# Kernel optimization log

Hardware: AMD Instinct MI355X
Metric: run time of the kernel (lower is better)

Reference implementation:

```python
import jax, jax.numpy as jnp
import numpy as np

IN_F = 4096
OUT_F = 4096
SPARSITY = 0.1
BATCH = 8192
TOTAL_PERM = max(IN_F, OUT_F)
DIAG_LEN = min(IN_F, OUT_F)
K = int(np.ceil((1.0 - SPARSITY) * IN_F * OUT_F / DIAG_LEN))  # 3687


def setup_inputs() -> dict:
    key = jax.random.key(0)
    k1, k2, k3 = jax.random.split(key, 3)
    x = jax.random.normal(k1, (BATCH, IN_F), dtype=jnp.float32)
    # kaiming_uniform_(a=sqrt(5)) on (TOTAL_PERM, DIAG_LEN): bound = 1/sqrt(fan_in)
    bound = 1.0 / np.sqrt(DIAG_LEN)
    V = jax.random.uniform(k2, (TOTAL_PERM, DIAG_LEN), jnp.float32, -bound, bound)
    # original init is constant 1/in_features; add small noise so soft top-k is non-trivial
    alpha = 1.0 / IN_F + 0.01 * jax.random.normal(k3, (TOTAL_PERM,), jnp.float32)
    return {"x": x, "V": V, "alpha": alpha}


def _compute_weight(V, alpha):
    # soft top-k: k * softmax(alpha / T), T=1, clamped to [0,1]; softmax > 0 so all
    # total_permutations diagonals participate (matches torch.nonzero behavior).
    a_topk = jnp.clip(K * jax.nn.softmax(alpha), 0.0, 1.0)  # [TOTAL_PERM]
    Vs = V * a_topk[:, None]  # [TOTAL_PERM, DIAG_LEN]
    d = jnp.arange(DIAG_LEN)
    # out_features >= in_features branch: diagonal i occupies rows (i+j)%out, cols j
    rows = (jnp.arange(TOTAL_PERM)[:, None] + d[None, :]) % OUT_F  # [N, D]
    cols = jnp.broadcast_to(d[None, :], (TOTAL_PERM, DIAG_LEN))
    W = jnp.zeros((OUT_F, IN_F), dtype=V.dtype).at[rows, cols].add(Vs)
    return W


def reference(x, V, alpha):
    W = _compute_weight(V, alpha)  # [OUT_F, IN_F]
    return x @ W.T  # F.linear(x, W)
```

## Files before the change

### kernel.cpp

```cpp
#include <hip/hip_runtime.h>

#define IN_F 4096
#define OUT_F 4096
#define BATCH 8192
#define KTOP 3687.0f

typedef float f32x4 __attribute__((ext_vector_type(4)));
typedef short bf16x8 __attribute__((ext_vector_type(8)));
typedef unsigned short ushort8 __attribute__((ext_vector_type(8)));

typedef __attribute__((address_space(1))) void gvoid;
typedef __attribute__((address_space(3))) void lvoid;

__device__ __forceinline__ unsigned short f2bf(float f) {
    unsigned int u = __float_as_uint(f);
    u += 0x7fff + ((u >> 16) & 1);
    return (unsigned short)(u >> 16);
}

__global__ __launch_bounds__(256) void atopk_kernel(const float* __restrict__ alpha,
                                                    float* __restrict__ atopk) {
    __shared__ float smax[4], ssum[4];
    int tid = threadIdx.x;
    float m = -1e30f;
    for (int i = tid; i < OUT_F; i += 256) m = fmaxf(m, alpha[i]);
    for (int o = 1; o < 64; o <<= 1) m = fmaxf(m, __shfl_xor(m, o));
    if ((tid & 63) == 0) smax[tid >> 6] = m;
    __syncthreads();
    m = fmaxf(fmaxf(smax[0], smax[1]), fmaxf(smax[2], smax[3]));
    float s = 0.f;
    for (int i = tid; i < OUT_F; i += 256) s += expf(alpha[i] - m);
    for (int o = 1; o < 64; o <<= 1) s += __shfl_xor(s, o);
    if ((tid & 63) == 0) ssum[tid >> 6] = s;
    __syncthreads();
    s = ssum[0] + ssum[1] + ssum[2] + ssum[3];
    float inv = 1.0f / s;
    for (int i = tid; i < OUT_F; i += 256) {
        float v = KTOP * expf(alpha[i] - m) * inv;
        atopk[i] = fminf(fmaxf(v, 0.0f), 1.0f);
    }
}

__global__ __launch_bounds__(256) void build_w_kernel(const float* __restrict__ V,
                                                      const float* __restrict__ atopk,
                                                      unsigned short* __restrict__ W) {
    int tx = threadIdx.x & 63;
    int ty = threadIdx.x >> 6;
    int c  = blockIdx.x * 64 + tx;
    int r0 = blockIdx.y * 64;
    #pragma unroll
    for (int it = 0; it < 16; ++it) {
        int r = r0 + it * 4 + ty;
        int s = (r - c) & (OUT_F - 1);
        float v = V[s * IN_F + c] * atopk[s];
        W[(long)r * IN_F + c] = f2bf(v);
    }
}

__global__ __launch_bounds__(256) void cvt_x_kernel(const float* __restrict__ x,
                                                    unsigned short* __restrict__ xb) {
    long i = ((long)blockIdx.x * 256 + threadIdx.x) * 8;
    const float* p = x + i;
    ushort8 o;
    #pragma unroll
    for (int j = 0; j < 8; ++j) o[j] = f2bf(p[j]);
    *(ushort8*)(xb + i) = o;
}

__global__ __launch_bounds__(256) void gemm_kernel(const unsigned short* __restrict__ A,
                                                   const unsigned short* __restrict__ Bt,
                                                   float* __restrict__ C) {
    __shared__ unsigned short As[2][128][32];
    __shared__ unsigned short Bs[2][128][32];

    const int tid = threadIdx.x;
    const int w = tid >> 6;
    const int l = tid & 63;
    const int wr = w >> 1, wc = w & 1;
    const int bn = blockIdx.x, bm = blockIdx.y;

    f32x4 acc[4][4] = {};

    const int srow = l >> 2;
    const int scol = (l & 3) * 8;
    const unsigned short* Abase = A  + ((long)bm * 128) * IN_F;
    const unsigned short* Bbase = Bt + ((long)bn * 128) * IN_F;

    const int lr = l & 15;
    const int lk = (l >> 4) * 8;

    for (int k0 = 0; k0 < IN_F; k0 += 64) {
        #pragma unroll
        for (int i = 0; i < 4; ++i) {
            int q = w * 4 + i;
            int h = q >> 3;
            int row = (q & 7) * 16 + srow;
            int kc = k0 + h * 32 + scol;
            __builtin_amdgcn_global_load_lds((gvoid*)(Abase + (long)row * IN_F + kc),
                                             (lvoid*)(&As[0][0][0] + q * 512), 16, 0, 0);
            __builtin_amdgcn_global_load_lds((gvoid*)(Bbase + (long)row * IN_F + kc),
                                             (lvoid*)(&Bs[0][0][0] + q * 512), 16, 0, 0);
        }
        __syncthreads();

        #pragma unroll
        for (int kk = 0; kk < 2; ++kk) {
            bf16x8 af[4], bfr[4];
            #pragma unroll
            for (int m = 0; m < 4; ++m)
                af[m] = *(const bf16x8*)(&As[kk][wr * 64 + m * 16 + lr][lk]);
            #pragma unroll
            for (int n = 0; n < 4; ++n)
                bfr[n] = *(const bf16x8*)(&Bs[kk][wc * 64 + n * 16 + lr][lk]);
            #pragma unroll
            for (int m = 0; m < 4; ++m)
                #pragma unroll
                for (int n = 0; n < 4; ++n)
                    acc[m][n] = __builtin_amdgcn_mfma_f32_16x16x32_bf16(af[m], bfr[n], acc[m][n], 0, 0, 0);
        }
        __syncthreads();
    }

    const long r0 = (long)bm * 128 + wr * 64;
    const int  c0 = bn * 128 + wc * 64;
    const int  rq = (l >> 4) * 4;
    #pragma unroll
    for (int m = 0; m < 4; ++m)
        #pragma unroll
        for (int n = 0; n < 4; ++n)
            #pragma unroll
            for (int v = 0; v < 4; ++v)
                C[(r0 + m * 16 + rq + v) * OUT_F + (c0 + n * 16 + lr)] = acc[m][n][v];
}

extern "C" void kernel_launch(void* const* d_in, const int* in_sizes, int n_in,
                              void* d_out, int out_size, void* d_ws, size_t ws_size,
                              hipStream_t stream) {
    const float* x     = (const float*)d_in[0];
    const float* V     = (const float*)d_in[1];
    const float* alpha = (const float*)d_in[2];
    float* out = (float*)d_out;

    char* ws = (char*)d_ws;
    float* atopk      = (float*)ws;
    unsigned short* W  = (unsigned short*)(ws + 16384);
    unsigned short* Xb = (unsigned short*)(ws + 16384 + (size_t)OUT_F * IN_F * 2);

    atopk_kernel<<<1, 256, 0, stream>>>(alpha, atopk);
    build_w_kernel<<<dim3(IN_F / 64, OUT_F / 64), 256, 0, stream>>>(V, atopk, W);
    cvt_x_kernel<<<(BATCH * IN_F / 8) / 256, 256, 0, stream>>>(x, Xb);
    gemm_kernel<<<dim3(OUT_F / 128, BATCH / 128), 256, 0, stream>>>(Xb, W, out);
}
```

Baseline: 634.4 us.

## Enlarge GEMM tiles to 256x256 with swizzled LDS and double-buffered prefetch

The GEMM moves from 128x128 tiles with 4 waves to 256x256 tiles with 8 waves and a K-step of 64. It uses an XOR-swizzled LDS layout to avoid bank conflicts, double-buffered asynchronous global-to-LDS loads with explicit vmcnt waits, and s_setprio around the MFMA bursts. The build_w kernel also stages a diagonal band of V in shared memory so its reads are coalesced instead of strided. The bigger tiles cut global traffic per FLOP and overlap loads with compute, at the cost of heavy LDS use (128KB) and register pressure from 32 accumulators, which limits occupancy.

Measured after the change: 547.9 us. -13.6%, faster.

```diff
diff --git a/kernel.cpp b/kernel.cpp
--- a/kernel.cpp
+++ b/kernel.cpp
@@ -4,6 +4,7 @@
 #define OUT_F 4096
 #define BATCH 8192
 #define KTOP 3687.0f
+#define NT (IN_F / 64)
 
 typedef float f32x4 __attribute__((ext_vector_type(4)));
 typedef short bf16x8 __attribute__((ext_vector_type(8)));
@@ -44,16 +45,29 @@
 __global__ __launch_bounds__(256) void build_w_kernel(const float* __restrict__ V,
                                                       const float* __restrict__ atopk,
                                                       unsigned short* __restrict__ W) {
-    int tx = threadIdx.x & 63;
-    int ty = threadIdx.x >> 6;
-    int c  = blockIdx.x * 64 + tx;
-    int r0 = blockIdx.y * 64;
+    __shared__ float Vl[128][64];
+    __shared__ float al[128];
+    const int t = threadIdx.x;
+    const int tx = t & 63, ty = t >> 6;
+    const int c0 = blockIdx.x * 64;
+    const int r0 = blockIdx.y * 64;
+    const int s_base = (r0 - c0 - 63 + 4096) & 4095;
+
+    #pragma unroll
+    for (int i = 0; i < 32; ++i) {
+        int sr = i * 4 + ty;
+        int gs = (s_base + sr) & 4095;
+        Vl[sr][tx] = V[(long)gs * IN_F + c0 + tx];
+    }
+    if (t < 128) al[t] = atopk[(s_base + t) & 4095];
+    __syncthreads();
+
     #pragma unroll
     for (int it = 0; it < 16; ++it) {
-        int r = r0 + it * 4 + ty;
-        int s = (r - c) & (OUT_F - 1);
-        float v = V[s * IN_F + c] * atopk[s];
-        W[(long)r * IN_F + c] = f2bf(v);
+        int ry = it * 4 + ty;
+        int si = ry - tx + 63;
+        float v = Vl[si][tx] * al[si];
+        W[(long)(r0 + ry) * IN_F + c0 + tx] = f2bf(v);
     }
 }
 
@@ -67,70 +81,126 @@
     *(ushort8*)(xb + i) = o;
 }
 
-__global__ __launch_bounds__(256) void gemm_kernel(const unsigned short* __restrict__ A,
-                                                   const unsigned short* __restrict__ Bt,
-                                                   float* __restrict__ C) {
-    __shared__ unsigned short As[2][128][32];
-    __shared__ unsigned short Bs[2][128][32];
+__global__ __launch_bounds__(512, 2) void gemm_kernel(const unsigned short* __restrict__ A,
+                                                      const unsigned short* __restrict__ Bt,
+                                                      float* __restrict__ C) {
+    __shared__ unsigned short As[2][256][64];
+    __shared__ unsigned short Bs[2][256][64];
 
     const int tid = threadIdx.x;
-    const int w = tid >> 6;
-    const int l = tid & 63;
-    const int wr = w >> 1, wc = w & 1;
+    const int l  = tid & 63;
+    const int w  = tid >> 6;
+    const int wr = w >> 2;
+    const int wc = w & 3;
+    const int lr = l & 15;
+    const int kq = l >> 4;
+    const int swz = (lr & 7) << 3;
+
     const int bn = blockIdx.x, bm = blockIdx.y;
 
-    f32x4 acc[4][4] = {};
-
-    const int srow = l >> 2;
-    const int scol = (l & 3) * 8;
-    const unsigned short* Abase = A  + ((long)bm * 128) * IN_F;
-    const unsigned short* Bbase = Bt + ((long)bn * 128) * IN_F;
-
-    const int lr = l & 15;
-    const int lk = (l >> 4) * 8;
-
-    for (int k0 = 0; k0 < IN_F; k0 += 64) {
-        #pragma unroll
-        for (int i = 0; i < 4; ++i) {
-            int q = w * 4 + i;
-            int h = q >> 3;
-            int row = (q & 7) * 16 + srow;
-            int kc = k0 + h * 32 + scol;
-            __builtin_amdgcn_global_load_lds((gvoid*)(Abase + (long)row * IN_F + kc),
-                                             (lvoid*)(&As[0][0][0] + q * 512), 16, 0, 0);
-            __builtin_amdgcn_global_load_lds((gvoid*)(Bbase + (long)row * IN_F + kc),
-                                             (lvoid*)(&Bs[0][0][0] + q * 512), 16, 0, 0);
-        }
-        __syncthreads();
-
-        #pragma unroll
-        for (int kk = 0; kk < 2; ++kk) {
-            bf16x8 af[4], bfr[4];
-            #pragma unroll
-            for (int m = 0; m < 4; ++m)
-                af[m] = *(const bf16x8*)(&As[kk][wr * 64 + m * 16 + lr][lk]);
-            #pragma unroll
-            for (int n = 0; n < 4; ++n)
-                bfr[n] = *(const bf16x8*)(&Bs[kk][wc * 64 + n * 16 + lr][lk]);
-            #pragma unroll
-            for (int m = 0; m < 4; ++m)
-                #pragma unroll
-                for (int n = 0; n < 4; ++n)
-                    acc[m][n] = __builtin_amdgcn_mfma_f32_16x16x32_bf16(af[m], bfr[n], acc[m][n], 0, 0, 0);
-        }
-        __syncthreads();
-    }
-
-    const long r0 = (long)bm * 128 + wr * 64;
-    const int  c0 = bn * 128 + wc * 64;
-    const int  rq = (l >> 4) * 4;
-    #pragma unroll
-    for (int m = 0; m < 4; ++m)
+    const unsigned short* Ab = A  + (long)bm * 256 * IN_F;
+    const unsigned short* Bb = Bt + (long)bn * 256 * IN_F;
+
+    const int srow = tid >> 3;
+    const int schunk = (tid & 7) ^ (srow & 7);
+    const int sdst = tid * 8;
+
+    f32x4 acc[8][4] = {};
+
+#define STAGE(kt, b) do {                                                          \
+    const unsigned short* ga_ = Ab + (long)(kt) * 64;                              \
+    const unsigned short* gb_ = Bb + (long)(kt) * 64;                              \
+    _Pragma("unroll")                                                              \
+    for (int j = 0; j < 4; ++j) {                                                  \
+        long r_ = (long)(j * 64 + srow);                                           \
+        __builtin_amdgcn_global_load_lds((gvoid*)(ga_ + r_ * IN_F + schunk * 8),   \
+            (lvoid*)(&As[b][0][0] + j * 4096 + sdst), 16, 0, 0);                   \
+    }                                                                              \
+    _Pragma("unroll")                                                              \
+    for (int j = 0; j < 4; ++j) {                                                  \
+        long r_ = (long)(j * 64 + srow);                                           \
+        __builtin_amdgcn_global_load_lds((gvoid*)(gb_ + r_ * IN_F + schunk * 8),   \
+            (lvoid*)(&Bs[b][0][0] + j * 4096 + sdst), 16, 0, 0);                   \
+    }                                                                              \
+} while (0)
+
+#define COMPUTE_TILE(b) do {                                                       \
+    const unsigned short (*Asb)[64] = As[b];                                       \
+    const unsigned short (*Bsb)[64] = Bs[b];                                       \
+    bf16x8 aA[4][2], bB[4][2];                                                     \
+    _Pragma("unroll")                                                              \
+    for (int n = 0; n < 4; ++n)                                                    \
+      _Pragma("unroll")                                                            \
+      for (int kk = 0; kk < 2; ++kk)                                               \
+        bB[n][kk] = *(const bf16x8*)&Bsb[wc * 64 + n * 16 + lr]                    \
+                                       [(kk * 32 + kq * 8) ^ swz];                 \
+    _Pragma("unroll")                                                              \
+    for (int m = 0; m < 4; ++m)                                                    \
+      _Pragma("unroll")                                                            \
+      for (int kk = 0; kk < 2; ++kk)                                               \
+        aA[m][kk] = *(const bf16x8*)&Asb[wr * 128 + m * 16 + lr]                   \
+                                        [(kk * 32 + kq * 8) ^ swz];                \
+    __builtin_amdgcn_s_setprio(1);                                                 \
+    _Pragma("unroll")                                                              \
+    for (int m = 0; m < 4; ++m)                                                    \
+      _Pragma("unroll")                                                            \
+      for (int n = 0; n < 4; ++n)                                                  \
+        _Pragma("unroll")                                                          \
+        for (int kk = 0; kk < 2; ++kk)                                             \
+          acc[m][n] = __builtin_amdgcn_mfma_f32_16x16x32_bf16(aA[m][kk], bB[n][kk],\
+                                                              acc[m][n], 0, 0, 0); \
+    __builtin_amdgcn_s_setprio(0);                                                 \
+    _Pragma("unroll")                                                              \
+    for (int m = 0; m < 4; ++m)                                                    \
+      _Pragma("unroll")                                                            \
+      for (int kk = 0; kk < 2; ++kk)                                               \
+        aA[m][kk] = *(const bf16x8*)&Asb[wr * 128 + (m + 4) * 16 + lr]             \
+                                        [(kk * 32 + kq * 8) ^ swz];                \
+    __builtin_amdgcn_s_setprio(1);                                                 \
+    _Pragma("unroll")                                                              \
+    for (int m = 0; m < 4; ++m)                                                    \
+      _Pragma("unroll")                                                            \
+      for (int n = 0; n < 4; ++n)                                                  \
+        _Pragma("unroll")                                                          \
+        for (int kk = 0; kk < 2; ++kk)                                             \
+          acc[m + 4][n] = __builtin_amdgcn_mfma_f32_16x16x32_bf16(aA[m][kk],       \
+                                          bB[n][kk], acc[m + 4][n], 0, 0, 0);      \
+    __builtin_amdgcn_s_setprio(0);                                                 \
+} while (0)
+
+    STAGE(0, 0);
+    STAGE(1, 1);
+    asm volatile("s_waitcnt vmcnt(8)" ::: "memory");
+    __builtin_amdgcn_s_barrier();
+
+    for (int t = 0; t < NT - 2; ++t) {
+        const int b = t & 1;
+        COMPUTE_TILE(b);
+        asm volatile("s_waitcnt lgkmcnt(0)" ::: "memory");
+        __builtin_amdgcn_s_barrier();
+        STAGE(t + 2, b);
+        asm volatile("s_waitcnt vmcnt(8)" ::: "memory");
+        __builtin_amdgcn_s_barrier();
+    }
+    COMPUTE_TILE(0);
+    asm volatile("s_waitcnt lgkmcnt(0)" ::: "memory");
+    __builtin_amdgcn_s_barrier();
+    asm volatile("s_waitcnt vmcnt(0)" ::: "memory");
+    __builtin_amdgcn_s_barrier();
+    COMPUTE_TILE(1);
+
+    const long r0 = (long)bm * 256 + wr * 128;
+    const int  c0 = bn * 256 + wc * 64;
+    const int  rq = kq * 4;
+    #pragma unroll
+    for (int m = 0; m < 8; ++m)
         #pragma unroll
         for (int n = 0; n < 4; ++n)
             #pragma unroll
             for (int v = 0; v < 4; ++v)
                 C[(r0 + m * 16 + rq + v) * OUT_F + (c0 + n * 16 + lr)] = acc[m][n][v];
+#undef STAGE
+#undef COMPUTE_TILE
 }
 
 extern "C" void kernel_launch(void* const* d_in, const int* in_sizes, int n_in,
@@ -149,5 +219,5 @@
     atopk_kernel<<<1, 256, 0, stream>>>(alpha, atopk);
     build_w_kernel<<<dim3(IN_F / 64, OUT_F / 64), 256, 0, stream>>>(V, atopk, W);
     cvt_x_kernel<<<(BATCH * IN_F / 8) / 256, 256, 0, stream>>>(x, Xb);
-    gemm_kernel<<<dim3(OUT_F / 128, BATCH / 128), 256, 0, stream>>>(Xb, W, out);
-}
+    gemm_kernel<<<dim3(OUT_F / 256, BATCH / 256), 512, 0, stream>>>(Xb, W, out);
+}
```
